# Optimization experiments

Hardware: AMD Instinct MI355X
Metric: run time of the kernel (lower is better)

Reference implementation:

```python
import jax, jax.numpy as jnp
import numpy as np

D_MODEL = 1024
D_FF = 4 * D_MODEL
NUM_EXPERTS = 8
TOP_K = 2


def setup_inputs() -> dict:
    key = jax.random.key(0)
    ks = jax.random.split(key, 7)
    B, S = 2, 2048
    x = jax.random.normal(ks[0], (B, S, D_MODEL), dtype=jnp.float32)
    s = 0.02
    Wr = jax.random.normal(ks[1], (D_MODEL, NUM_EXPERTS), dtype=jnp.float32) * s
    br = jnp.zeros((NUM_EXPERTS,), dtype=jnp.float32)
    W1 = jax.random.normal(ks[2], (NUM_EXPERTS, D_MODEL, D_FF), dtype=jnp.float32) * s
    b1 = jnp.zeros((NUM_EXPERTS, D_FF), dtype=jnp.float32)
    W2 = jax.random.normal(ks[3], (NUM_EXPERTS, D_FF, D_MODEL), dtype=jnp.float32) * s
    b2 = jnp.zeros((NUM_EXPERTS, D_MODEL), dtype=jnp.float32)
    return {"x": x, "Wr": Wr, "br": br, "W1": W1, "b1": b1, "W2": W2, "b2": b2}


def reference(x, Wr, br, W1, b1, W2, b2):
    E, K = NUM_EXPERTS, TOP_K
    # Router: softmax over experts, hard top-k gating, renormalize.
    gate_logits = jnp.einsum('bsd,de->bse', x, Wr) + br  # [B,S,E]
    gate_probs = jax.nn.softmax(gate_logits, axis=-1)
    topk_vals, topk_idx = jax.lax.top_k(gate_probs, K)  # [B,S,K]
    oh = jax.nn.one_hot(topk_idx, E, dtype=gate_probs.dtype)  # [B,S,K,E]
    hard = jnp.einsum('bske,bsk->bse', oh, topk_vals)  # scattered top-k probs
    hard = hard / jnp.clip(hard.sum(axis=-1, keepdims=True), 1e-9)
    # Dense per-expert FFN (every expert sees all tokens, as in the source).
    h = jnp.einsum('bsd,edh->ebsh', x, W1) + b1[:, None, None, :]  # [E,B,S,4D]
    h = jax.nn.gelu(h, approximate=False)  # torch nn.GELU default = exact erf
    y = jnp.einsum('ebsh,ehd->ebsd', h, W2) + b2[:, None, None, :]  # [E,B,S,D]
    output = jnp.einsum('ebsd,bse->bsd', y, hard)
    # Aux load-balancing loss (no mask branch).
    flat_probs = gate_probs.reshape(-1, E)
    assignments = jnp.argmax(flat_probs, axis=-1)
    f = jnp.mean(jax.nn.one_hot(assignments, E, dtype=flat_probs.dtype), axis=0)
    P = flat_probs.mean(axis=0)
    aux_loss = E * jnp.sum(f * P)
    return output, aux_loss
```

## Files before the change

kernel.cpp:

```cpp
#include <hip/hip_runtime.h>
#include <cstdint>
#include <cstddef>

#define NTOK 4096
#define DM   1024
#define DFF  4096
#define NE   8
#define MAXTILES 72

typedef __attribute__((ext_vector_type(8))) __bf16 bf16x8;
typedef __attribute__((ext_vector_type(4))) float  f32x4;

__device__ __forceinline__ unsigned short f2bf(float f) {
  union { float f; unsigned int u; } c; c.f = f;
  unsigned int u = c.u;
  return (unsigned short)((u + 0x7fffu + ((u >> 16) & 1u)) >> 16);
}

__device__ __forceinline__ void async16(const void* g, void* l) {
  __builtin_amdgcn_global_load_lds(
      (const __attribute__((address_space(1))) void*)(uintptr_t)g,
      (__attribute__((address_space(3))) void*)(uint32_t)(uintptr_t)l,
      16, 0, 0);
}

__device__ __forceinline__ float gelu_erf(float v) {
  float u = v * 0.70710678118f;
  float az = fabsf(u);
  float t = __builtin_amdgcn_rcpf(fmaf(0.3275911f, az, 1.f));
  float p = fmaf(1.061405429f, t, -1.453152027f);
  p = fmaf(p, t, 1.421413741f);
  p = fmaf(p, t, -0.284496736f);
  p = fmaf(p, t, 0.254829592f);
  p = p * t;
  float ex = __builtin_amdgcn_exp2f(-az * az * 1.44269504089f);
  float er = fmaf(-p, ex, 1.f);
  er = copysignf(er, u);
  return 0.5f * v * (1.f + er);
}

__global__ void k_cvt_x(const float* __restrict__ x, unsigned short* __restrict__ xb) {
  int i = (blockIdx.x * 256 + threadIdx.x) * 4;
  float4 v = *(const float4*)(x + i);
  ushort4 o;
  o.x = f2bf(v.x); o.y = f2bf(v.y); o.z = f2bf(v.z); o.w = f2bf(v.w);
  *(ushort4*)(xb + i) = o;
}

__global__ void k_transpose_bf(const float* __restrict__ src, unsigned short* __restrict__ dst,
                               int R, int C) {
  __shared__ float tile[32][33];
  int e = blockIdx.z;
  src += (size_t)e * R * C;
  dst += (size_t)e * R * C;
  int tx = threadIdx.x, ty = threadIdx.y;
  int c = blockIdx.x * 32 + tx;
#pragma unroll
  for (int q = 0; q < 4; q++) {
    int r = blockIdx.y * 32 + q * 8 + ty;
    tile[q * 8 + ty][tx] = src[(size_t)r * C + c];
  }
  __syncthreads();
#pragma unroll
  for (int q = 0; q < 4; q++) {
    dst[(size_t)(blockIdx.x * 32 + q * 8 + ty) * R + blockIdx.y * 32 + tx] =
        f2bf(tile[tx][q * 8 + ty]);
  }
}

__global__ void k_router(const float* __restrict__ x, const float* __restrict__ Wr,
                         const float* __restrict__ br, int* __restrict__ cnt,
                         int* __restrict__ fcnt, float* __restrict__ Psum,
                         int* __restrict__ toklist, float* __restrict__ wlist,
                         int* __restrict__ tokmap, float* __restrict__ tokw) {
  __shared__ float sP[NE];
  __shared__ int sF[NE];
  int tid = threadIdx.x;
  if (tid < NE) { sP[tid] = 0.f; sF[tid] = 0; }
  __syncthreads();
  int tok = blockIdx.x * 32 + (tid >> 3);
  int e = tid & 7;
  const float* xr = x + (size_t)tok * DM;
  float acc = 0.f;
#pragma unroll 4
  for (int i = 0; i < DM; i += 4) {
    float4 xv = *(const float4*)(xr + i);
    acc = fmaf(xv.x, Wr[(i + 0) * NE + e], acc);
    acc = fmaf(xv.y, Wr[(i + 1) * NE + e], acc);
    acc = fmaf(xv.z, Wr[(i + 2) * NE + e], acc);
    acc = fmaf(xv.w, Wr[(i + 3) * NE + e], acc);
  }
  acc += br[e];
  float m = acc;
  for (int s = 1; s < 8; s <<= 1) m = fmaxf(m, __shfl_xor(m, s));
  float p = expf(acc - m);
  float sum = p;
  for (int s = 1; s < 8; s <<= 1) sum += __shfl_xor(sum, s);
  float prob = p / sum;
  atomicAdd(&sP[e], prob);
  int lanebase = (tid & 63) & ~7;
  float pv[8];
#pragma unroll
  for (int j = 0; j < 8; j++) pv[j] = __shfl(prob, lanebase + j);
  if (e == 0) {
    int i1 = 0; float v1 = pv[0];
#pragma unroll
    for (int j = 1; j < 8; j++) if (pv[j] > v1) { v1 = pv[j]; i1 = j; }
    int i2 = -1; float v2 = -1.f;
#pragma unroll
    for (int j = 0; j < 8; j++) if (j != i1 && pv[j] > v2) { v2 = pv[j]; i2 = j; }
    float inv = 1.f / (v1 + v2);
    int s1 = atomicAdd(&cnt[i1], 1);
    toklist[i1 * NTOK + s1] = tok; wlist[i1 * NTOK + s1] = v1 * inv;
    int s2 = atomicAdd(&cnt[i2], 1);
    toklist[i2 * NTOK + s2] = tok; wlist[i2 * NTOK + s2] = v2 * inv;
    tokmap[tok * 2] = (i1 << 16) | s1;  tokw[tok * 2] = v1 * inv;
    tokmap[tok * 2 + 1] = (i2 << 16) | s2; tokw[tok * 2 + 1] = v2 * inv;
    atomicAdd(&sF[i1], 1);
  }
  __syncthreads();
  if (tid < NE) { atomicAdd(&Psum[tid], sP[tid]); atomicAdd(&fcnt[tid], sF[tid]); }
}

__global__ void k_scan_aux(const int* __restrict__ cnt, const int* __restrict__ fcnt,
                           const float* __restrict__ Psum, int* __restrict__ offs,
                           int* __restrict__ ntiles, int* __restrict__ tileE,
                           int* __restrict__ tileM0, float* __restrict__ aux_out) {
  if (threadIdx.x == 0) {
    int o = 0; float a = 0.f; int t = 0;
    for (int e = 0; e < NE; e++) {
      offs[e] = o; o += cnt[e];
      a += (float)fcnt[e] * Psum[e];
      for (int m0 = 0; m0 < cnt[e]; m0 += 128) { tileE[t] = e; tileM0[t] = m0; t++; }
    }
    *ntiles = t;
    aux_out[0] = 8.f * a / (4096.f * 4096.f);
  }
}

__global__ __launch_bounds__(256) void k_ffn1(
    const unsigned short* __restrict__ xb, const unsigned short* __restrict__ w1t,
    const float* __restrict__ b1, const int* __restrict__ cnt,
    const int* __restrict__ offs, const int* __restrict__ ntiles,
    const int* __restrict__ tileE, const int* __restrict__ tileM0,
    const int* __restrict__ toklist, unsigned short* __restrict__ H) {
  int t = blockIdx.y;
  if (t >= *ntiles) return;
  int e = tileE[t], m0 = tileM0[t];
  int cn = cnt[e];
  int n0 = blockIdx.x * 128;
  __shared__ __align__(16) unsigned short At[128 * 64];
  __shared__ __align__(16) unsigned short Bt[128 * 64];
  int tid = threadIdx.x;
  int chunk = tid & 7, rsub = tid >> 3;
  int cg = (chunk ^ (rsub & 7)) * 8;
  const unsigned short* gA[4]; const unsigned short* gB[4];
  unsigned short* lA[4]; unsigned short* lB[4];
#pragma unroll
  for (int q = 0; q < 4; q++) {
    int row = q * 32 + rsub;
    int tr = m0 + row; if (tr >= cn) tr = cn - 1;
    int tok = toklist[e * NTOK + tr];
    gA[q] = xb + (size_t)tok * DM + cg;
    gB[q] = w1t + ((size_t)e * DFF + n0 + row) * DM + cg;
    lA[q] = At + row * 64 + chunk * 8;
    lB[q] = Bt + row * 64 + chunk * 8;
  }
  int wid = tid >> 6, lane = tid & 63;
  int mW = (wid >> 1) * 64, nW = (wid & 1) * 64;
  int lr = lane & 15, quad = lane >> 4;
  int sw = lane & 7;
  f32x4 acc[4][4];
#pragma unroll
  for (int i = 0; i < 4; i++)
#pragma unroll
    for (int j = 0; j < 4; j++) acc[i][j] = (f32x4)(0.f);
  for (int k0 = 0; k0 < DM; k0 += 64) {
#pragma unroll
    for (int q = 0; q < 4; q++) async16(gA[q] + k0, lA[q]);
#pragma unroll
    for (int q = 0; q < 4; q++) async16(gB[q] + k0, lB[q]);
    __syncthreads();
#pragma unroll
    for (int kk8 = 0; kk8 < 8; kk8 += 4) {
      int cs = ((kk8 + quad) ^ sw) * 8;
      bf16x8 a[4], b[4];
#pragma unroll
      for (int i = 0; i < 4; i++) a[i] = *(const bf16x8*)(At + (mW + i * 16 + lr) * 64 + cs);
#pragma unroll
      for (int j = 0; j < 4; j++) b[j] = *(const bf16x8*)(Bt + (nW + j * 16 + lr) * 64 + cs);
#pragma unroll
      for (int i = 0; i < 4; i++)
#pragma unroll
        for (int j = 0; j < 4; j++)
          acc[i][j] = __builtin_amdgcn_mfma_f32_16x16x32_bf16(a[i], b[j], acc[i][j], 0, 0, 0);
    }
    __syncthreads();
  }
  int off = offs[e];
#pragma unroll
  for (int i = 0; i < 4; i++) {
#pragma unroll
    for (int r = 0; r < 4; r++) {
      int gr = m0 + mW + i * 16 + quad * 4 + r;
      if (gr < cn) {
        size_t base = (size_t)(off + gr) * DFF + n0;
#pragma unroll
        for (int j = 0; j < 4; j++) {
          int col = nW + j * 16 + lr;
          float v = acc[i][j][r] + b1[(size_t)e * DFF + n0 + col];
          H[base + col] = f2bf(gelu_erf(v));
        }
      }
    }
  }
}

__global__ __launch_bounds__(256) void k_ffn2(
    const unsigned short* __restrict__ H, const unsigned short* __restrict__ w2t,
    const int* __restrict__ cnt, const int* __restrict__ offs,
    const int* __restrict__ ntiles, const int* __restrict__ tileE,
    const int* __restrict__ tileM0, float* __restrict__ P) {
  int t = blockIdx.y;
  if (t >= *ntiles) return;
  int e = tileE[t], m0 = tileM0[t];
  int cn = cnt[e];
  int n0 = blockIdx.x * 128;
  int kz = blockIdx.z;
  int off = offs[e];
  __shared__ __align__(16) unsigned short At[128 * 64];
  __shared__ __align__(16) unsigned short Bt[128 * 64];
  int tid = threadIdx.x;
  int chunk = tid & 7, rsub = tid >> 3;
  int cg = (chunk ^ (rsub & 7)) * 8;
  const unsigned short* gA[4]; const unsigned short* gB[4];
  unsigned short* lA[4]; unsigned short* lB[4];
#pragma unroll
  for (int q = 0; q < 4; q++) {
    int row = q * 32 + rsub;
    int hr = m0 + row; if (hr >= cn) hr = cn - 1;
    gA[q] = H + (size_t)(off + hr) * DFF + cg;
    gB[q] = w2t + ((size_t)e * DM + n0 + row) * DFF + cg;
    lA[q] = At + row * 64 + chunk * 8;
    lB[q] = Bt + row * 64 + chunk * 8;
  }
  int wid = tid >> 6, lane = tid & 63;
  int mW = (wid >> 1) * 64, nW = (wid & 1) * 64;
  int lr = lane & 15, quad = lane >> 4;
  int sw = lane & 7;
  f32x4 acc[4][4];
#pragma unroll
  for (int i = 0; i < 4; i++)
#pragma unroll
    for (int j = 0; j < 4; j++) acc[i][j] = (f32x4)(0.f);
  int kbeg = kz * (DFF / 2), kend = kbeg + DFF / 2;
  for (int k0 = kbeg; k0 < kend; k0 += 64) {
#pragma unroll
    for (int q = 0; q < 4; q++) async16(gA[q] + k0, lA[q]);
#pragma unroll
    for (int q = 0; q < 4; q++) async16(gB[q] + k0, lB[q]);
    __syncthreads();
#pragma unroll
    for (int kk8 = 0; kk8 < 8; kk8 += 4) {
      int cs = ((kk8 + quad) ^ sw) * 8;
      bf16x8 a[4], b[4];
#pragma unroll
      for (int i = 0; i < 4; i++) a[i] = *(const bf16x8*)(At + (mW + i * 16 + lr) * 64 + cs);
#pragma unroll
      for (int j = 0; j < 4; j++) b[j] = *(const bf16x8*)(Bt + (nW + j * 16 + lr) * 64 + cs);
#pragma unroll
      for (int i = 0; i < 4; i++)
#pragma unroll
        for (int j = 0; j < 4; j++)
          acc[i][j] = __builtin_amdgcn_mfma_f32_16x16x32_bf16(a[i], b[j], acc[i][j], 0, 0, 0);
    }
    __syncthreads();
  }
  float* Pk = P + (size_t)kz * 8192 * DM;
#pragma unroll
  for (int i = 0; i < 4; i++) {
#pragma unroll
    for (int r = 0; r < 4; r++) {
      int gr = m0 + mW + i * 16 + quad * 4 + r;
      if (gr < cn) {
        size_t base = (size_t)(off + gr) * DM + n0;
#pragma unroll
        for (int j = 0; j < 4; j++) {
          int col = nW + j * 16 + lr;
          Pk[base + col] = acc[i][j][r];
        }
      }
    }
  }
}

__global__ __launch_bounds__(256) void k_combine(
    const float* __restrict__ P, const float* __restrict__ b2,
    const int* __restrict__ offs, const int* __restrict__ tokmap,
    const float* __restrict__ tokw, float* __restrict__ out) {
  int tok = blockIdx.x;
  int c4 = threadIdx.x * 4;
  int enc0 = tokmap[tok * 2], enc1 = tokmap[tok * 2 + 1];
  float w0 = tokw[tok * 2], w1 = tokw[tok * 2 + 1];
  int e0 = enc0 >> 16, p0 = enc0 & 0xffff;
  int e1 = enc1 >> 16, p1 = enc1 & 0xffff;
  size_t r0 = (size_t)(offs[e0] + p0) * DM;
  size_t r1 = (size_t)(offs[e1] + p1) * DM;
  const size_t KZ = (size_t)8192 * DM;
  float4 a0 = *(const float4*)(P + r0 + c4);
  float4 a1 = *(const float4*)(P + KZ + r0 + c4);
  float4 c0 = *(const float4*)(P + r1 + c4);
  float4 c1 = *(const float4*)(P + KZ + r1 + c4);
  float4 bb0 = *(const float4*)(b2 + (size_t)e0 * DM + c4);
  float4 bb1 = *(const float4*)(b2 + (size_t)e1 * DM + c4);
  float4 o;
  o.x = w0 * (a0.x + a1.x + bb0.x) + w1 * (c0.x + c1.x + bb1.x);
  o.y = w0 * (a0.y + a1.y + bb0.y) + w1 * (c0.y + c1.y + bb1.y);
  o.z = w0 * (a0.z + a1.z + bb0.z) + w1 * (c0.z + c1.z + bb1.z);
  o.w = w0 * (a0.w + a1.w + bb0.w) + w1 * (c0.w + c1.w + bb1.w);
  *(float4*)(out + (size_t)tok * DM + c4) = o;
}

__global__ void k_wsfail(float* out, float v) { if (threadIdx.x == 0) out[0] = v; }

extern "C" void kernel_launch(void* const* d_in, const int* in_sizes, int n_in,
                              void* d_out, int out_size, void* d_ws, size_t ws_size,
                              hipStream_t stream) {
  const float* x  = (const float*)d_in[0];
  const float* Wr = (const float*)d_in[1];
  const float* br = (const float*)d_in[2];
  const float* W1 = (const float*)d_in[3];
  const float* b1 = (const float*)d_in[4];
  const float* W2 = (const float*)d_in[5];
  const float* b2 = (const float*)d_in[6];
  float* out = (float*)d_out;
  char* ws = (char*)d_ws;

  const size_t NEED = ((size_t)144 << 20) + (size_t)8192 * DFF * 2;
  if (ws_size < NEED) {
    hipLaunchKernelGGL(k_wsfail, dim3(1), dim3(64), 0, stream, out, (float)ws_size);
    return;
  }
  int* cnt      = (int*)(ws + 0);
  int* fcnt     = (int*)(ws + 64);
  float* Psum   = (float*)(ws + 128);
  int* offs     = (int*)(ws + 192);
  int* ntiles   = (int*)(ws + 256);
  int* tileE    = (int*)(ws + 512);
  int* tileM0   = (int*)(ws + 1024);
  int* toklist  = (int*)(ws + 4096);
  float* wlist  = (float*)(ws + 135168);
  int* tokmap   = (int*)(ws + 266240);
  float* tokw   = (float*)(ws + 299008);
  unsigned short* xb  = (unsigned short*)(ws + ((size_t)1 << 20));
  unsigned short* w1t = (unsigned short*)(ws + ((size_t)10 << 20));
  float*          Pp  = (float*)(ws + ((size_t)10 << 20));
  unsigned short* w2t = (unsigned short*)(ws + ((size_t)80 << 20));
  unsigned short* Hb  = (unsigned short*)(ws + ((size_t)144 << 20));

  hipMemsetAsync(ws, 0, 4096, stream);

  hipLaunchKernelGGL(k_cvt_x, dim3(NTOK * DM / 1024), dim3(256), 0, stream, x, xb);
  hipLaunchKernelGGL(k_transpose_bf, dim3(DFF / 32, DM / 32, NE), dim3(32, 8), 0, stream, W1, w1t, DM, DFF);
  hipLaunchKernelGGL(k_transpose_bf, dim3(DM / 32, DFF / 32, NE), dim3(32, 8), 0, stream, W2, w2t, DFF, DM);
  hipLaunchKernelGGL(k_router, dim3(NTOK / 32), dim3(256), 0, stream, x, Wr, br, cnt, fcnt, Psum,
                     toklist, wlist, tokmap, tokw);
  hipLaunchKernelGGL(k_scan_aux, dim3(1), dim3(64), 0, stream, cnt, fcnt, Psum, offs, ntiles, tileE, tileM0, out + (out_size - 1));
  hipLaunchKernelGGL(k_ffn1, dim3(DFF / 128, MAXTILES), dim3(256), 0, stream,
                     xb, w1t, b1, cnt, offs, ntiles, tileE, tileM0, toklist, Hb);
  hipLaunchKernelGGL(k_ffn2, dim3(DM / 128, MAXTILES, 2), dim3(256), 0, stream,
                     Hb, w2t, cnt, offs, ntiles, tileE, tileM0, Pp);
  hipLaunchKernelGGL(k_combine, dim3(NTOK), dim3(256), 0, stream,
                     Pp, b2, offs, tokmap, tokw, out);
}
```

Measured before the change: 652.2 us.

## Double-buffer GEMM LDS tiles, widen weight transpose, fuse x cast into router

Both FFN GEMM kernels now use two LDS buffers, so the next K-slice is loaded asynchronously while MFMAs run on the current one, and one barrier per iteration is removed. The weight transpose-and-cast kernel moves to 64x64 tiles with float4 loads and ushort4 stores to cut memory transactions. The separate x-to-bf16 kernel is dropped and the cast is folded into the router kernel, which already reads x. Doubling LDS per block may reduce occupancy, and with a single barrier per iteration the async-load wait semantics are a correctness risk.

```diff
diff --git a/kernel.cpp b/kernel.cpp
--- a/kernel.cpp
+++ b/kernel.cpp
@@ -7,6 +7,7 @@
 #define DFF  4096
 #define NE   8
 #define MAXTILES 72
+#define BUFS 8192
 
 typedef __attribute__((ext_vector_type(8))) __bf16 bf16x8;
 typedef __attribute__((ext_vector_type(4))) float  f32x4;
@@ -39,32 +40,32 @@
   return 0.5f * v * (1.f + er);
 }
 
-__global__ void k_cvt_x(const float* __restrict__ x, unsigned short* __restrict__ xb) {
-  int i = (blockIdx.x * 256 + threadIdx.x) * 4;
-  float4 v = *(const float4*)(x + i);
-  ushort4 o;
-  o.x = f2bf(v.x); o.y = f2bf(v.y); o.z = f2bf(v.z); o.w = f2bf(v.w);
-  *(ushort4*)(xb + i) = o;
-}
-
-__global__ void k_transpose_bf(const float* __restrict__ src, unsigned short* __restrict__ dst,
-                               int R, int C) {
-  __shared__ float tile[32][33];
+__global__ __launch_bounds__(256) void k_transpose_bf(const float* __restrict__ src,
+                                                      unsigned short* __restrict__ dst,
+                                                      int R, int C) {
+  __shared__ float tile[64][65];
   int e = blockIdx.z;
   src += (size_t)e * R * C;
   dst += (size_t)e * R * C;
-  int tx = threadIdx.x, ty = threadIdx.y;
-  int c = blockIdx.x * 32 + tx;
+  int lx = threadIdx.x & 15, ly = threadIdx.x >> 4;
+  int c0 = blockIdx.x * 64, r0 = blockIdx.y * 64;
 #pragma unroll
   for (int q = 0; q < 4; q++) {
-    int r = blockIdx.y * 32 + q * 8 + ty;
-    tile[q * 8 + ty][tx] = src[(size_t)r * C + c];
+    int r = q * 16 + ly;
+    float4 v = *(const float4*)(src + (size_t)(r0 + r) * C + c0 + lx * 4);
+    tile[r][lx * 4 + 0] = v.x; tile[r][lx * 4 + 1] = v.y;
+    tile[r][lx * 4 + 2] = v.z; tile[r][lx * 4 + 3] = v.w;
   }
   __syncthreads();
 #pragma unroll
   for (int q = 0; q < 4; q++) {
-    dst[(size_t)(blockIdx.x * 32 + q * 8 + ty) * R + blockIdx.y * 32 + tx] =
-        f2bf(tile[tx][q * 8 + ty]);
+    int cc = q * 16 + ly;
+    ushort4 o;
+    o.x = f2bf(tile[lx * 4 + 0][cc]);
+    o.y = f2bf(tile[lx * 4 + 1][cc]);
+    o.z = f2bf(tile[lx * 4 + 2][cc]);
+    o.w = f2bf(tile[lx * 4 + 3][cc]);
+    *(ushort4*)(dst + (size_t)(c0 + cc) * R + r0 + lx * 4) = o;
   }
 }
 
@@ -72,7 +73,8 @@
                          const float* __restrict__ br, int* __restrict__ cnt,
                          int* __restrict__ fcnt, float* __restrict__ Psum,
                          int* __restrict__ toklist, float* __restrict__ wlist,
-                         int* __restrict__ tokmap, float* __restrict__ tokw) {
+                         int* __restrict__ tokmap, float* __restrict__ tokw,
+                         unsigned short* __restrict__ xb) {
   __shared__ float sP[NE];
   __shared__ int sF[NE];
   int tid = threadIdx.x;
@@ -91,6 +93,13 @@
     acc = fmaf(xv.w, Wr[(i + 3) * NE + e], acc);
   }
   acc += br[e];
+#pragma unroll 4
+  for (int j = 0; j < 32; j++) {
+    int idx = e * 4 + j * 32;
+    float4 v = *(const float4*)(xr + idx);
+    ushort4 o; o.x = f2bf(v.x); o.y = f2bf(v.y); o.z = f2bf(v.z); o.w = f2bf(v.w);
+    *(ushort4*)(xb + (size_t)tok * DM + idx) = o;
+  }
   float m = acc;
   for (int s = 1; s < 8; s <<= 1) m = fmaxf(m, __shfl_xor(m, s));
   float p = expf(acc - m);
@@ -149,8 +158,8 @@
   int e = tileE[t], m0 = tileM0[t];
   int cn = cnt[e];
   int n0 = blockIdx.x * 128;
-  __shared__ __align__(16) unsigned short At[128 * 64];
-  __shared__ __align__(16) unsigned short Bt[128 * 64];
+  __shared__ __align__(16) unsigned short At[2 * BUFS];
+  __shared__ __align__(16) unsigned short Bt[2 * BUFS];
   int tid = threadIdx.x;
   int chunk = tid & 7, rsub = tid >> 3;
   int cg = (chunk ^ (rsub & 7)) * 8;
@@ -175,27 +184,37 @@
   for (int i = 0; i < 4; i++)
 #pragma unroll
     for (int j = 0; j < 4; j++) acc[i][j] = (f32x4)(0.f);
-  for (int k0 = 0; k0 < DM; k0 += 64) {
-#pragma unroll
-    for (int q = 0; q < 4; q++) async16(gA[q] + k0, lA[q]);
-#pragma unroll
-    for (int q = 0; q < 4; q++) async16(gB[q] + k0, lB[q]);
+#pragma unroll
+  for (int q = 0; q < 4; q++) async16(gA[q], lA[q]);
+#pragma unroll
+  for (int q = 0; q < 4; q++) async16(gB[q], lB[q]);
+  const int NK = DM / 64;
+  for (int k0 = 0; k0 < NK; k0++) {
     __syncthreads();
+    if (k0 + 1 < NK) {
+      int koff = (k0 + 1) * 64;
+      int nb = ((k0 + 1) & 1) * BUFS;
+#pragma unroll
+      for (int q = 0; q < 4; q++) async16(gA[q] + koff, lA[q] + nb);
+#pragma unroll
+      for (int q = 0; q < 4; q++) async16(gB[q] + koff, lB[q] + nb);
+    }
+    const unsigned short* Ab = At + (k0 & 1) * BUFS;
+    const unsigned short* Bb = Bt + (k0 & 1) * BUFS;
 #pragma unroll
     for (int kk8 = 0; kk8 < 8; kk8 += 4) {
       int cs = ((kk8 + quad) ^ sw) * 8;
       bf16x8 a[4], b[4];
 #pragma unroll
-      for (int i = 0; i < 4; i++) a[i] = *(const bf16x8*)(At + (mW + i * 16 + lr) * 64 + cs);
-#pragma unroll
-      for (int j = 0; j < 4; j++) b[j] = *(const bf16x8*)(Bt + (nW + j * 16 + lr) * 64 + cs);
+      for (int i = 0; i < 4; i++) a[i] = *(const bf16x8*)(Ab + (mW + i * 16 + lr) * 64 + cs);
+#pragma unroll
+      for (int j = 0; j < 4; j++) b[j] = *(const bf16x8*)(Bb + (nW + j * 16 + lr) * 64 + cs);
 #pragma unroll
       for (int i = 0; i < 4; i++)
 #pragma unroll
         for (int j = 0; j < 4; j++)
           acc[i][j] = __builtin_amdgcn_mfma_f32_16x16x32_bf16(a[i], b[j], acc[i][j], 0, 0, 0);
     }
-    __syncthreads();
   }
   int off = offs[e];
 #pragma unroll
@@ -228,19 +247,20 @@
   int n0 = blockIdx.x * 128;
   int kz = blockIdx.z;
   int off = offs[e];
-  __shared__ __align__(16) unsigned short At[128 * 64];
-  __shared__ __align__(16) unsigned short Bt[128 * 64];
+  __shared__ __align__(16) unsigned short At[2 * BUFS];
+  __shared__ __align__(16) unsigned short Bt[2 * BUFS];
   int tid = threadIdx.x;
   int chunk = tid & 7, rsub = tid >> 3;
   int cg = (chunk ^ (rsub & 7)) * 8;
   const unsigned short* gA[4]; const unsigned short* gB[4];
   unsigned short* lA[4]; unsigned short* lB[4];
+  int kbeg = kz * (DFF / 2);
 #pragma unroll
   for (int q = 0; q < 4; q++) {
     int row = q * 32 + rsub;
     int hr = m0 + row; if (hr >= cn) hr = cn - 1;
-    gA[q] = H + (size_t)(off + hr) * DFF + cg;
-    gB[q] = w2t + ((size_t)e * DM + n0 + row) * DFF + cg;
+    gA[q] = H + (size_t)(off + hr) * DFF + kbeg + cg;
+    gB[q] = w2t + ((size_t)e * DM + n0 + row) * DFF + kbeg + cg;
     lA[q] = At + row * 64 + chunk * 8;
     lB[q] = Bt + row * 64 + chunk * 8;
   }
@@ -253,28 +273,37 @@
   for (int i = 0; i < 4; i++)
 #pragma unroll
     for (int j = 0; j < 4; j++) acc[i][j] = (f32x4)(0.f);
-  int kbeg = kz * (DFF / 2), kend = kbeg + DFF / 2;
-  for (int k0 = kbeg; k0 < kend; k0 += 64) {
-#pragma unroll
-    for (int q = 0; q < 4; q++) async16(gA[q] + k0, lA[q]);
-#pragma unroll
-    for (int q = 0; q < 4; q++) async16(gB[q] + k0, lB[q]);
+#pragma unroll
+  for (int q = 0; q < 4; q++) async16(gA[q], lA[q]);
+#pragma unroll
+  for (int q = 0; q < 4; q++) async16(gB[q], lB[q]);
+  const int NK = (DFF / 2) / 64;
+  for (int k0 = 0; k0 < NK; k0++) {
     __syncthreads();
+    if (k0 + 1 < NK) {
+      int koff = (k0 + 1) * 64;
+      int nb = ((k0 + 1) & 1) * BUFS;
+#pragma unroll
+      for (int q = 0; q < 4; q++) async16(gA[q] + koff, lA[q] + nb);
+#pragma unroll
+      for (int q = 0; q < 4; q++) async16(gB[q] + koff, lB[q] + nb);
+    }
+    const unsigned short* Ab = At + (k0 & 1) * BUFS;
+    const unsigned short* Bb = Bt + (k0 & 1) * BUFS;
 #pragma unroll
     for (int kk8 = 0; kk8 < 8; kk8 += 4) {
       int cs = ((kk8 + quad) ^ sw) * 8;
       bf16x8 a[4], b[4];
 #pragma unroll
-      for (int i = 0; i < 4; i++) a[i] = *(const bf16x8*)(At + (mW + i * 16 + lr) * 64 + cs);
-#pragma unroll
-      for (int j = 0; j < 4; j++) b[j] = *(const bf16x8*)(Bt + (nW + j * 16 + lr) * 64 + cs);
+      for (int i = 0; i < 4; i++) a[i] = *(const bf16x8*)(Ab + (mW + i * 16 + lr) * 64 + cs);
+#pragma unroll
+      for (int j = 0; j < 4; j++) b[j] = *(const bf16x8*)(Bb + (nW + j * 16 + lr) * 64 + cs);
 #pragma unroll
       for (int i = 0; i < 4; i++)
 #pragma unroll
         for (int j = 0; j < 4; j++)
           acc[i][j] = __builtin_amdgcn_mfma_f32_16x16x32_bf16(a[i], b[j], acc[i][j], 0, 0, 0);
     }
-    __syncthreads();
   }
   float* Pk = P + (size_t)kz * 8192 * DM;
 #pragma unroll
@@ -360,11 +389,10 @@
 
   hipMemsetAsync(ws, 0, 4096, stream);
 
-  hipLaunchKernelGGL(k_cvt_x, dim3(NTOK * DM / 1024), dim3(256), 0, stream, x, xb);
-  hipLaunchKernelGGL(k_transpose_bf, dim3(DFF / 32, DM / 32, NE), dim3(32, 8), 0, stream, W1, w1t, DM, DFF);
-  hipLaunchKernelGGL(k_transpose_bf, dim3(DM / 32, DFF / 32, NE), dim3(32, 8), 0, stream, W2, w2t, DFF, DM);
+  hipLaunchKernelGGL(k_transpose_bf, dim3(DFF / 64, DM / 64, NE), dim3(256), 0, stream, W1, w1t, DM, DFF);
+  hipLaunchKernelGGL(k_transpose_bf, dim3(DM / 64, DFF / 64, NE), dim3(256), 0, stream, W2, w2t, DFF, DM);
   hipLaunchKernelGGL(k_router, dim3(NTOK / 32), dim3(256), 0, stream, x, Wr, br, cnt, fcnt, Psum,
-                     toklist, wlist, tokmap, tokw);
+                     toklist, wlist, tokmap, tokw, xb);
   hipLaunchKernelGGL(k_scan_aux, dim3(1), dim3(64), 0, stream, cnt, fcnt, Psum, offs, ntiles, tileE, tileM0, out + (out_size - 1));
   hipLaunchKernelGGL(k_ffn1, dim3(DFF / 128, MAXTILES), dim3(256), 0, stream,
                      xb, w1t, b1, cnt, offs, ntiles, tileE, tileM0, toklist, Hb);
```

Result: faster. 629.0 us (-3.6%).
